# Optimization experiments

Hardware: AMD Instinct MI355X
Metric: run time of the kernel (lower is better)

Reference implementation:

```python
import jax, jax.numpy as jnp
import numpy as np

ALPHA = 1.0  # initial_alpha; forward uses self.alpha which stays at init value

def setup_inputs() -> dict:
    key = jax.random.key(0)
    k1, k2, k3, k4 = jax.random.split(key, 4)
    B, T, N, C, K = 8, 32, 2048, 64, 32
    R_seq = jax.random.normal(k1, (B, T, N, C), dtype=jnp.float32)
    W = jax.random.normal(k2, (K, C), dtype=jnp.float32) * (1.0 / np.sqrt(C))
    b = jax.random.normal(k3, (K,), dtype=jnp.float32) * 0.01
    cent = jax.random.normal(k4, (K, C), dtype=jnp.float32)
    centroids = cent / jnp.linalg.norm(cent, axis=1, keepdims=True)  # xavier + L2-normalize rows
    return {"R_seq": R_seq, "W": W, "b": b, "centroids": centroids}

def reference(R_seq, W, b, centroids):
    B, T, N, C = R_seq.shape
    K = centroids.shape[0]
    r = R_seq.reshape(B * T, N, C)                       # (BT, N, C)
    logits = (jnp.einsum('mnc,kc->mnk', r, W) + b) * ALPHA
    a = jax.nn.softmax(logits, axis=-1)                  # (BT, N, K)
    # NetVLAD algebraic decomposition: v_k = a_k^T r - (sum_n a_nk) * c_k
    v = jnp.einsum('mnk,mnc->mkc', a, r) - a.sum(axis=1)[:, :, None] * centroids[None]
    return v.reshape(B, T, K, C)
```

## Files before the change

### kernel.cpp

```cpp
#include <hip/hip_runtime.h>
#include <stdint.h>

typedef __attribute__((ext_vector_type(8))) short bf16x8;
typedef __attribute__((ext_vector_type(4))) short bf16x4;
typedef __attribute__((ext_vector_type(4))) float f32x4;

#define NSPLIT 4
#define WAVES 4
#define STAGES 8
#define STAGE_FLOATS (16 * 64)
#define A_STRIDE 40
#define VB_STRIDE 68

static __device__ __forceinline__ unsigned short f2bf(float f) {
    union { float f; unsigned int i; } x; x.f = f;
    unsigned int i = x.i;
    return (unsigned short)((i + 0x7FFFu + ((i >> 16) & 1u)) >> 16);
}

static __device__ __forceinline__ bf16x8 cvt8(float4 a, float4 b) {
    bf16x8 r;
    r[0] = (short)f2bf(a.x); r[1] = (short)f2bf(a.y);
    r[2] = (short)f2bf(a.z); r[3] = (short)f2bf(a.w);
    r[4] = (short)f2bf(b.x); r[5] = (short)f2bf(b.y);
    r[6] = (short)f2bf(b.z); r[7] = (short)f2bf(b.w);
    return r;
}

static __device__ __forceinline__ float row_sum16(float x) {
    union fi { float f; int i; };
    fi a, b; a.f = x;
    b.i = __builtin_amdgcn_mov_dpp(a.i, 0x128, 0xf, 0xf, false); a.f += b.f;
    b.i = __builtin_amdgcn_mov_dpp(a.i, 0x124, 0xf, 0xf, false); a.f += b.f;
    b.i = __builtin_amdgcn_mov_dpp(a.i, 0x122, 0xf, 0xf, false); a.f += b.f;
    b.i = __builtin_amdgcn_mov_dpp(a.i, 0x121, 0xf, 0xf, false); a.f += b.f;
    return a.f;
}

static __device__ __forceinline__ void dma16(const float* g, float* l) {
    __builtin_amdgcn_global_load_lds(
        (const __attribute__((address_space(1))) void*)g,
        (__attribute__((address_space(3))) void*)l, 16, 0, 0);
}

__global__ __launch_bounds__(256, 3)
void netvlad_fused(const float* __restrict__ R,
                   const float* __restrict__ W,
                   const float* __restrict__ bias,
                   const float* __restrict__ cent,
                   float* __restrict__ out)
{
    __shared__ float dma[WAVES][2][STAGE_FLOATS];
    __shared__ short a_lds_s[WAVES][32 * A_STRIDE];
    __shared__ float suma_buf[2][32];

    const int tid  = threadIdx.x;
    const int wave = tid >> 6;
    const int lane = tid & 63;
    const int l15  = lane & 15;
    const int quad = lane >> 4;
    const int m    = blockIdx.x >> 2;
    const int q    = blockIdx.x & 3;

    const float* Rm  = R + (size_t)m * (2048 * 64);
    const int row0   = q * 512 + wave * 128;

    short* a_lds = a_lds_s[wave];
    float* buf0  = dma[wave][0];
    float* buf1  = dma[wave][1];

    bf16x8 wf[2][2];
#pragma unroll
    for (int kt = 0; kt < 2; ++kt)
#pragma unroll
        for (int cc = 0; cc < 2; ++cc) {
            const float* wp = W + (kt*16 + l15)*64 + cc*32 + quad*8;
            wf[kt][cc] = cvt8(*(const float4*)wp, *(const float4*)(wp + 4));
        }
    float bval[2];
    bval[0] = bias[l15];
    bval[1] = bias[16 + l15];

    f32x4 acc[2][4];
#pragma unroll
    for (int kt = 0; kt < 2; ++kt)
#pragma unroll
        for (int ct = 0; ct < 4; ++ct)
            acc[kt][ct] = (f32x4){0.f, 0.f, 0.f, 0.f};
    float suma[2] = {0.f, 0.f};

    {
        const float* src = Rm + (size_t)row0 * 64;
#pragma unroll
        for (int t = 0; t < 4; ++t)
            dma16(src + t*256 + lane*4, buf0 + t*256);
    }
    float4 cur[4];
    {
        const float* p = Rm + (size_t)row0*64 + l15*64 + quad*8;
        cur[0] = *(const float4*)p;        cur[1] = *(const float4*)(p + 4);
        cur[2] = *(const float4*)(p + 32); cur[3] = *(const float4*)(p + 36);
    }

#pragma unroll
    for (int s = 0; s < STAGES; ++s) {
        float* bufn = (s & 1) ? buf0 : buf1;
        const float* nsrc = Rm + (size_t)(row0 + (s+1)*16) * 64;

        if (!(s & 1) && s + 1 < STAGES) {
#pragma unroll
            for (int t = 0; t < 4; ++t)
                dma16(nsrc + t*256 + lane*4, bufn + t*256);
        }
        float4 nxt[4];
        if (s + 1 < STAGES) {
            const float* p = nsrc + l15*64 + quad*8;
            nxt[0] = *(const float4*)p;        nxt[1] = *(const float4*)(p + 4);
            nxt[2] = *(const float4*)(p + 32); nxt[3] = *(const float4*)(p + 36);
        }

        bf16x8 af0 = cvt8(cur[0], cur[1]);
        bf16x8 af1 = cvt8(cur[2], cur[3]);
        f32x4 d1[2];
#pragma unroll
        for (int kt = 0; kt < 2; ++kt) {
            f32x4 d = (f32x4){0.f, 0.f, 0.f, 0.f};
            d = __builtin_amdgcn_mfma_f32_16x16x32_bf16(af0, wf[kt][0], d, 0, 0, 0);
            d = __builtin_amdgcn_mfma_f32_16x16x32_bf16(af1, wf[kt][1], d, 0, 0, 0);
            d1[kt] = d;
        }

        bf16x4 p0, p1;
        float a0s = 0.f, a1s = 0.f;
#pragma unroll
        for (int r = 0; r < 4; ++r) {
            float l0 = d1[0][r] + bval[0];
            float l1 = d1[1][r] + bval[1];
            float e0 = __expf(l0);
            float e1 = __expf(l1);
            float ss = row_sum16(e0 + e1);
            float rs = __builtin_amdgcn_rcpf(ss);
            float a0 = e0 * rs, a1 = e1 * rs;
            a0s += a0; a1s += a1;
            p0[r] = (short)f2bf(a0);
            p1[r] = (short)f2bf(a1);
        }
        suma[0] += a0s; suma[1] += a1s;
        *(bf16x4*)(a_lds + l15*A_STRIDE        + (s&1)*16 + quad*4) = p0;
        *(bf16x4*)(a_lds + (16 + l15)*A_STRIDE + (s&1)*16 + quad*4) = p1;

        if (s & 1) {
            asm volatile("s_waitcnt vmcnt(4)" ::: "memory");

            bf16x8 a2[2];
            a2[0] = *(bf16x8*)(a_lds + l15*A_STRIDE        + quad*8);
            a2[1] = *(bf16x8*)(a_lds + (16 + l15)*A_STRIDE + quad*8);

            const float* bb = (quad < 2) ? buf0 : buf1;
            const float* bp = bb + (quad & 1) * 8 * 64 + l15;
#pragma unroll
            for (int ct = 0; ct < 4; ++ct) {
                const float* bq = bp + ct*16;
                bf16x8 b2;
#pragma unroll
                for (int j = 0; j < 8; ++j)
                    b2[j] = (short)f2bf(bq[j*64]);
                acc[0][ct] = __builtin_amdgcn_mfma_f32_16x16x32_bf16(a2[0], b2, acc[0][ct], 0, 0, 0);
                acc[1][ct] = __builtin_amdgcn_mfma_f32_16x16x32_bf16(a2[1], b2, acc[1][ct], 0, 0, 0);
            }
            if (s + 1 < STAGES) {
#pragma unroll
                for (int t = 0; t < 4; ++t)
                    dma16(nsrc + t*256 + lane*4, bufn + t*256);
            }
        }

        if (s + 1 < STAGES) {
            cur[0] = nxt[0]; cur[1] = nxt[1]; cur[2] = nxt[2]; cur[3] = nxt[3];
        }
    }

#pragma unroll
    for (int kt = 0; kt < 2; ++kt) {
        suma[kt] += __shfl_xor(suma[kt], 16);
        suma[kt] += __shfl_xor(suma[kt], 32);
    }

    float* vbuf = (float*)dma;
    __syncthreads();
    if (wave >= 2) {
        float* dst = vbuf + (wave - 2) * (32 * VB_STRIDE);
#pragma unroll
        for (int kt = 0; kt < 2; ++kt)
#pragma unroll
            for (int ct = 0; ct < 4; ++ct)
#pragma unroll
                for (int r = 0; r < 4; ++r)
                    dst[(kt*16 + quad*4 + r)*VB_STRIDE + ct*16 + l15] = acc[kt][ct][r];
        if (lane < 16) {
            suma_buf[wave - 2][lane]      = suma[0];
            suma_buf[wave - 2][lane + 16] = suma[1];
        }
    }
    __syncthreads();
    if (wave < 2) {
        const float* src = vbuf + wave * (32 * VB_STRIDE);
#pragma unroll
        for (int kt = 0; kt < 2; ++kt)
#pragma unroll
            for (int ct = 0; ct < 4; ++ct)
#pragma unroll
                for (int r = 0; r < 4; ++r)
                    acc[kt][ct][r] += src[(kt*16 + quad*4 + r)*VB_STRIDE + ct*16 + l15];
        suma[0] += suma_buf[wave][l15];
        suma[1] += suma_buf[wave][l15 + 16];
    }
    __syncthreads();
    if (wave == 1) {
#pragma unroll
        for (int kt = 0; kt < 2; ++kt)
#pragma unroll
            for (int ct = 0; ct < 4; ++ct)
#pragma unroll
                for (int r = 0; r < 4; ++r)
                    vbuf[(kt*16 + quad*4 + r)*VB_STRIDE + ct*16 + l15] = acc[kt][ct][r];
        if (lane < 16) {
            suma_buf[0][lane]      = suma[0];
            suma_buf[0][lane + 16] = suma[1];
        }
    }
    __syncthreads();
    if (wave == 0) {
#pragma unroll
        for (int kt = 0; kt < 2; ++kt)
#pragma unroll
            for (int ct = 0; ct < 4; ++ct)
#pragma unroll
                for (int r = 0; r < 4; ++r)
                    acc[kt][ct][r] += vbuf[(kt*16 + quad*4 + r)*VB_STRIDE + ct*16 + l15];
        suma[0] += suma_buf[0][l15];
        suma[1] += suma_buf[0][l15 + 16];

        float* op = out + (size_t)m * (32*64);
#pragma unroll
        for (int kt = 0; kt < 2; ++kt) {
#pragma unroll
            for (int r = 0; r < 4; ++r) {
                const int k = kt*16 + quad*4 + r;
                const float su = __shfl(suma[kt], quad*4 + r);
#pragma unroll
                for (int ct = 0; ct < 4; ++ct) {
                    const int c = ct*16 + l15;
                    atomicAdd(&op[k*64 + c], acc[kt][ct][r] - su * cent[k*64 + c]);
                }
            }
        }
    }
}

extern "C" void kernel_launch(void* const* d_in, const int* in_sizes, int n_in,
                              void* d_out, int out_size, void* d_ws, size_t ws_size,
                              hipStream_t stream) {
    (void)in_sizes; (void)n_in; (void)out_size; (void)d_ws; (void)ws_size;
    const float* R = (const float*)d_in[0];
    const float* W = (const float*)d_in[1];
    const float* b = (const float*)d_in[2];
    const float* c = (const float*)d_in[3];
    float* out = (float*)d_out;

    hipMemsetAsync(out, 0, (size_t)256 * 32 * 64 * sizeof(float), stream);
    hipLaunchKernelGGL(netvlad_fused, dim3(256 * NSPLIT), dim3(256), 0, stream,
                       R, W, b, c, out);
}
```

Baseline: 216.8 us.

## Replace LDS DMA staging with register-converted bf16 transposed tile in LDS

New measurement: 250.5 us. 15.5% more time.

```diff
diff --git a/kernel.cpp b/kernel.cpp
--- a/kernel.cpp
+++ b/kernel.cpp
@@ -5,12 +5,10 @@
 typedef __attribute__((ext_vector_type(4))) short bf16x4;
 typedef __attribute__((ext_vector_type(4))) float f32x4;
 
-#define NSPLIT 4
-#define WAVES 4
-#define STAGES 8
-#define STAGE_FLOATS (16 * 64)
-#define A_STRIDE 40
+#define RT_STRIDE 40
+#define A_STRIDE  40
 #define VB_STRIDE 68
+#define WAVE_SHORTS (64*RT_STRIDE + 32*A_STRIDE)
 
 static __device__ __forceinline__ unsigned short f2bf(float f) {
     union { float f; unsigned int i; } x; x.f = f;
@@ -37,21 +35,14 @@
     return a.f;
 }
 
-static __device__ __forceinline__ void dma16(const float* g, float* l) {
-    __builtin_amdgcn_global_load_lds(
-        (const __attribute__((address_space(1))) void*)g,
-        (__attribute__((address_space(3))) void*)l, 16, 0, 0);
-}
-
-__global__ __launch_bounds__(256, 3)
+__global__ __launch_bounds__(256, 4)
 void netvlad_fused(const float* __restrict__ R,
                    const float* __restrict__ W,
                    const float* __restrict__ bias,
                    const float* __restrict__ cent,
                    float* __restrict__ out)
 {
-    __shared__ float dma[WAVES][2][STAGE_FLOATS];
-    __shared__ short a_lds_s[WAVES][32 * A_STRIDE];
+    __shared__ short smem[4 * WAVE_SHORTS];
     __shared__ float suma_buf[2][32];
 
     const int tid  = threadIdx.x;
@@ -62,12 +53,11 @@
     const int m    = blockIdx.x >> 2;
     const int q    = blockIdx.x & 3;
 
-    const float* Rm  = R + (size_t)m * (2048 * 64);
-    const int row0   = q * 512 + wave * 128;
-
-    short* a_lds = a_lds_s[wave];
-    float* buf0  = dma[wave][0];
-    float* buf1  = dma[wave][1];
+    const float* Rm = R + (size_t)m * (2048 * 64);
+    const int row0  = q * 512 + wave * 128;
+
+    short* rt    = smem + wave * WAVE_SHORTS;
+    short* a_lds = rt + 64 * RT_STRIDE;
 
     bf16x8 wf[2][2];
 #pragma unroll
@@ -89,38 +79,25 @@
             acc[kt][ct] = (f32x4){0.f, 0.f, 0.f, 0.f};
     float suma[2] = {0.f, 0.f};
 
-    {
-        const float* src = Rm + (size_t)row0 * 64;
-#pragma unroll
-        for (int t = 0; t < 4; ++t)
-            dma16(src + t*256 + lane*4, buf0 + t*256);
-    }
     float4 cur[4];
     {
-        const float* p = Rm + (size_t)row0*64 + l15*64 + quad*8;
+        const float* p = Rm + (size_t)(row0 + l15)*64 + quad*8;
         cur[0] = *(const float4*)p;        cur[1] = *(const float4*)(p + 4);
         cur[2] = *(const float4*)(p + 32); cur[3] = *(const float4*)(p + 36);
     }
 
 #pragma unroll
-    for (int s = 0; s < STAGES; ++s) {
-        float* bufn = (s & 1) ? buf0 : buf1;
-        const float* nsrc = Rm + (size_t)(row0 + (s+1)*16) * 64;
-
-        if (!(s & 1) && s + 1 < STAGES) {
-#pragma unroll
-            for (int t = 0; t < 4; ++t)
-                dma16(nsrc + t*256 + lane*4, bufn + t*256);
-        }
+    for (int s = 0; s < 8; ++s) {
         float4 nxt[4];
-        if (s + 1 < STAGES) {
-            const float* p = nsrc + l15*64 + quad*8;
+        if (s < 7) {
+            const float* p = Rm + (size_t)(row0 + (s+1)*16 + l15)*64 + quad*8;
             nxt[0] = *(const float4*)p;        nxt[1] = *(const float4*)(p + 4);
             nxt[2] = *(const float4*)(p + 32); nxt[3] = *(const float4*)(p + 36);
         }
 
         bf16x8 af0 = cvt8(cur[0], cur[1]);
         bf16x8 af1 = cvt8(cur[2], cur[3]);
+
         f32x4 d1[2];
 #pragma unroll
         for (int kt = 0; kt < 2; ++kt) {
@@ -134,50 +111,46 @@
         float a0s = 0.f, a1s = 0.f;
 #pragma unroll
         for (int r = 0; r < 4; ++r) {
-            float l0 = d1[0][r] + bval[0];
-            float l1 = d1[1][r] + bval[1];
-            float e0 = __expf(l0);
-            float e1 = __expf(l1);
-            float ss = row_sum16(e0 + e1);
-            float rs = __builtin_amdgcn_rcpf(ss);
+            float e0 = __expf(d1[0][r] + bval[0]);
+            float e1 = __expf(d1[1][r] + bval[1]);
+            float rs = __builtin_amdgcn_rcpf(row_sum16(e0 + e1));
             float a0 = e0 * rs, a1 = e1 * rs;
             a0s += a0; a1s += a1;
             p0[r] = (short)f2bf(a0);
             p1[r] = (short)f2bf(a1);
         }
         suma[0] += a0s; suma[1] += a1s;
-        *(bf16x4*)(a_lds + l15*A_STRIDE        + (s&1)*16 + quad*4) = p0;
-        *(bf16x4*)(a_lds + (16 + l15)*A_STRIDE + (s&1)*16 + quad*4) = p1;
+
+        const int nwin = (s & 1) * 16;
+        *(bf16x4*)(a_lds + l15*A_STRIDE        + nwin + quad*4) = p0;
+        *(bf16x4*)(a_lds + (16 + l15)*A_STRIDE + nwin + quad*4) = p1;
+
+        {
+            const int nsw = (nwin + l15) ^ (quad << 3);
+            short* base0 = rt + (quad*8) * RT_STRIDE + nsw;
+            short* base1 = rt + (32 + quad*8) * RT_STRIDE + nsw;
+#pragma unroll
+            for (int e = 0; e < 8; ++e) {
+                base0[e * RT_STRIDE] = af0[e];
+                base1[e * RT_STRIDE] = af1[e];
+            }
+        }
 
         if (s & 1) {
-            asm volatile("s_waitcnt vmcnt(4)" ::: "memory");
-
             bf16x8 a2[2];
             a2[0] = *(bf16x8*)(a_lds + l15*A_STRIDE        + quad*8);
             a2[1] = *(bf16x8*)(a_lds + (16 + l15)*A_STRIDE + quad*8);
 
-            const float* bb = (quad < 2) ? buf0 : buf1;
-            const float* bp = bb + (quad & 1) * 8 * 64 + l15;
 #pragma unroll
             for (int ct = 0; ct < 4; ++ct) {
-                const float* bq = bp + ct*16;
-                bf16x8 b2;
-#pragma unroll
-                for (int j = 0; j < 8; ++j)
-                    b2[j] = (short)f2bf(bq[j*64]);
+                const int v = (2*ct + (l15 >> 3)) & 3;
+                bf16x8 b2 = *(bf16x8*)(rt + (ct*16 + l15)*RT_STRIDE + 8*(quad ^ v));
                 acc[0][ct] = __builtin_amdgcn_mfma_f32_16x16x32_bf16(a2[0], b2, acc[0][ct], 0, 0, 0);
                 acc[1][ct] = __builtin_amdgcn_mfma_f32_16x16x32_bf16(a2[1], b2, acc[1][ct], 0, 0, 0);
             }
-            if (s + 1 < STAGES) {
-#pragma unroll
-                for (int t = 0; t < 4; ++t)
-                    dma16(nsrc + t*256 + lane*4, bufn + t*256);
-            }
-        }
-
-        if (s + 1 < STAGES) {
-            cur[0] = nxt[0]; cur[1] = nxt[1]; cur[2] = nxt[2]; cur[3] = nxt[3];
-        }
+        }
+
+        if (s < 7) { cur[0] = nxt[0]; cur[1] = nxt[1]; cur[2] = nxt[2]; cur[3] = nxt[3]; }
     }
 
 #pragma unroll
@@ -186,7 +159,7 @@
         suma[kt] += __shfl_xor(suma[kt], 32);
     }
 
-    float* vbuf = (float*)dma;
+    float* vbuf = (float*)smem;
     __syncthreads();
     if (wave >= 2) {
         float* dst = vbuf + (wave - 2) * (32 * VB_STRIDE);
@@ -269,6 +242,6 @@
     float* out = (float*)d_out;
 
     hipMemsetAsync(out, 0, (size_t)256 * 32 * 64 * sizeof(float), stream);
-    hipLaunchKernelGGL(netvlad_fused, dim3(256 * NSPLIT), dim3(256), 0, stream,
+    hipLaunchKernelGGL(netvlad_fused, dim3(1024), dim3(256), 0, stream,
                        R, W, b, c, out);
 }
```
